# Performance work log

Measured on AMD Instinct MI355X. Metric: run time of the kernel, lower is better.

## Reference

```python
import jax, jax.numpy as jnp
import numpy as np

HEADS = 8
DIM_HEAD = 64
DIM_COOR = 3
SCALE = (DIM_COOR * DIM_HEAD) ** -0.5


def setup_inputs() -> dict:
    key = jax.random.key(0)
    k1, k2, k3 = jax.random.split(key, 3)
    x = jax.random.normal(k1, (2, 2048, 256, 3), dtype=jnp.float32)
    w_qkv = jax.random.normal(k2, (1536, 256), dtype=jnp.float32)
    w_out = jax.random.normal(k3, (256, 512), dtype=jnp.float32)
    return {"x": x, "w_qkv": w_qkv, "w_out": w_out}


def reference(x, w_qkv, w_out):
    b, n, _, c = x.shape
    # VNLinear: contract feature dim, keep coord dim  -> [b, n, 3*h*d, c]
    qkv = jnp.einsum('bnic,oi->bnoc', x, w_qkv)
    q, k, v = jnp.split(qkv, 3, axis=-2)  # each [b, n, h*d, c]

    def to_heads(t):
        return t.reshape(b, n, HEADS, DIM_HEAD, c).transpose(0, 2, 1, 3, 4)  # b h n d c

    q, k, v = map(to_heads, (q, k, v))
    q = q * SCALE
    # scores sum over head-dim AND coordinate-dim
    sim = jnp.einsum('bhidc,bhjdc->bhij', q, k)
    attn = jax.nn.softmax(sim, axis=-1)
    out = jnp.einsum('bhij,bhjdc->bhidc', attn, v)  # coord dim preserved
    out = out.transpose(0, 2, 1, 3, 4).reshape(b, n, HEADS * DIM_HEAD, c)
    return jnp.einsum('bnic,oi->bnoc', out, w_out)
```

## Files before the change

kernel.cpp:

```cpp
#include <hip/hip_runtime.h>
#include <hip/hip_bf16.h>

#define SCALE 0.07216878364870322f
#define LOG2E 1.4426950408889634f

typedef __bf16 bf16x8 __attribute__((ext_vector_type(8)));
typedef float f32x16 __attribute__((ext_vector_type(16)));
typedef float f32x4v __attribute__((ext_vector_type(4)));
typedef unsigned int u32x4 __attribute__((ext_vector_type(4)));
typedef unsigned short u16;

#define MFMA(a, b, c) __builtin_amdgcn_mfma_f32_32x32x16_bf16(a, b, c, 0, 0, 0)
#define MFMA16(a, b, c) __builtin_amdgcn_mfma_f32_16x16x32_bf16(a, b, c, 0, 0, 0)

__device__ __forceinline__ u16 b16(float v) { return __builtin_bit_cast(u16, (__bf16)v); }
__device__ __forceinline__ float fb16(u16 u) {
    unsigned int t = (unsigned int)u << 16;
    return __builtin_bit_cast(float, t);
}
__device__ __forceinline__ unsigned int splitpack(float v) {
    u16 h = b16(v);
    float r = v - fb16(h);
    return (unsigned int)h | ((unsigned int)b16(r) << 16);
}
__device__ __forceinline__ unsigned int pack2(float a, float b) {
    return (unsigned int)b16(a) | ((unsigned int)b16(b) << 16);
}
__device__ __forceinline__ void gload16(const void* g, void* l) {
    __builtin_amdgcn_global_load_lds((const __attribute__((address_space(1))) void*)g,
                                     (__attribute__((address_space(3))) void*)l, 16, 0, 0);
}

__global__ __launch_bounds__(256) void qkv_mfma(const float* __restrict__ x,
                                                const float* __restrict__ wq,
                                                u16* __restrict__ Qhi, u16* __restrict__ Qlo,
                                                u16* __restrict__ KVf) {
    __shared__ unsigned int ldsr[2][32][196];
    const int tid = threadIdx.x;
    const int lane = tid & 63, w = tid >> 6, hf = lane >> 5, l31 = lane & 31;
    const int lq = lane & 15, gq = lane >> 4;
    const int o0 = blockIdx.x * 64;
    const int n0 = blockIdx.y * 128;
    const int b = blockIdx.z;
    const int nw0 = n0 + w * 32;
    const int part = o0 >> 9;
    const int h = (o0 >> 6) & 7;
    const int bh = b * 8 + h;

    const float* xp = x + ((size_t)(b * 2048 + nw0 + l31)) * 768 + hf * 24;
    const float* wp0 = wq + (size_t)(o0 + l31) * 256 + hf * 8;
    const float* wp1 = wp0 + 32 * 256;

    f32x16 acc[3][2] = {};
    #pragma unroll 2
    for (int k0 = 0; k0 < 16; ++k0) {
        float xf[24], wf0[8], wf1[8];
        #pragma unroll
        for (int q = 0; q < 6; ++q) {
            f32x4v t = *(const f32x4v*)(xp + k0 * 48 + q * 4);
            xf[q * 4 + 0] = t[0]; xf[q * 4 + 1] = t[1];
            xf[q * 4 + 2] = t[2]; xf[q * 4 + 3] = t[3];
        }
        {
            f32x4v t0 = *(const f32x4v*)(wp0 + k0 * 16);
            f32x4v t1 = *(const f32x4v*)(wp0 + k0 * 16 + 4);
            f32x4v t2 = *(const f32x4v*)(wp1 + k0 * 16);
            f32x4v t3 = *(const f32x4v*)(wp1 + k0 * 16 + 4);
            #pragma unroll
            for (int e = 0; e < 4; ++e) {
                wf0[e] = t0[e]; wf0[4 + e] = t1[e];
                wf1[e] = t2[e]; wf1[4 + e] = t3[e];
            }
        }
        bf16x8 xh[3], xl[3], wh[2], wl[2];
        #pragma unroll
        for (int c = 0; c < 3; ++c)
            #pragma unroll
            for (int e = 0; e < 8; ++e) {
                float v = xf[e * 3 + c];
                __bf16 hi = (__bf16)v;
                xh[c][e] = hi;
                xl[c][e] = (__bf16)(v - (float)hi);
            }
        #pragma unroll
        for (int e = 0; e < 8; ++e) {
            { float v = wf0[e]; __bf16 hi = (__bf16)v; wh[0][e] = hi; wl[0][e] = (__bf16)(v - (float)hi); }
            { float v = wf1[e]; __bf16 hi = (__bf16)v; wh[1][e] = hi; wl[1][e] = (__bf16)(v - (float)hi); }
        }
        #pragma unroll
        for (int c = 0; c < 3; ++c)
            #pragma unroll
            for (int ot = 0; ot < 2; ++ot) {
                acc[c][ot] = MFMA(xh[c], wh[ot], acc[c][ot]);
                acc[c][ot] = MFMA(xl[c], wh[ot], acc[c][ot]);
                acc[c][ot] = MFMA(xh[c], wl[ot], acc[c][ot]);
            }
    }

    #pragma unroll
    for (int round = 0; round < 2; ++round) {
        __syncthreads();
        if ((w >> 1) == round) {
            unsigned int (*L)[196] = ldsr[w & 1];
            #pragma unroll
            for (int c = 0; c < 3; ++c)
                #pragma unroll
                for (int ot = 0; ot < 2; ++ot)
                    #pragma unroll
                    for (int r = 0; r < 16; ++r) {
                        float v = acc[c][ot][r];
                        if (part == 0) v *= (SCALE * LOG2E);
                        int nn = (r & 3) + 8 * (r >> 2) + 4 * hf;
                        int dcol = 3 * (ot * 32 + l31) + c;
                        L[nn][dcol] = (part == 2) ? (unsigned int)b16(v) : splitpack(v);
                    }
            if (part < 2) {
                #pragma unroll
                for (int is = 0; is < 2; ++is)
                    #pragma unroll
                    for (int kc = 0; kc < 6; ++kc) {
                        const unsigned int* p = &L[is * 16 + lq][kc * 32 + gq * 8];
                        u32x4 a = *(const u32x4*)p;
                        u32x4 bq = *(const u32x4*)(p + 4);
                        u32x4 hi = { (a[0] & 0xffffu) | (a[1] << 16), (a[2] & 0xffffu) | (a[3] << 16),
                                     (bq[0] & 0xffffu) | (bq[1] << 16), (bq[2] & 0xffffu) | (bq[3] << 16) };
                        u32x4 lo = { (a[0] >> 16) | (a[1] & 0xffff0000u), (a[2] >> 16) | (a[3] & 0xffff0000u),
                                     (bq[0] >> 16) | (bq[1] & 0xffff0000u), (bq[2] >> 16) | (bq[3] & 0xffff0000u) };
                        if (part == 0) {
                            size_t off = ((size_t)(bh * 128 + (nw0 >> 4) + is) * 6 + kc) * 512 + lane * 8;
                            *(u32x4*)(Qhi + off) = hi;
                            *(u32x4*)(Qlo + off) = lo;
                        } else {
                            size_t off = (size_t)(bh * 64 + (nw0 >> 5)) * 18432 + (is * 6 + kc) * 512 + lane * 8;
                            *(u32x4*)(KVf + off) = hi;
                            *(u32x4*)(KVf + off + 6144) = lo;
                        }
                    }
            } else {
                u16* vp = KVf + (size_t)(bh * 64 + (nw0 >> 5)) * 18432 + 12288 + lane * 8;
                #pragma unroll
                for (int d = 0; d < 12; ++d) {
                    unsigned int t[8];
                    #pragma unroll
                    for (int e = 0; e < 8; ++e)
                        t[e] = L[gq * 8 + e][d * 16 + lq];
                    u32x4 pk = { (t[0] & 0xffffu) | (t[1] << 16), (t[2] & 0xffffu) | (t[3] << 16),
                                 (t[4] & 0xffffu) | (t[5] << 16), (t[6] & 0xffffu) | (t[7] << 16) };
                    *(u32x4*)(vp + d * 512) = pk;
                }
            }
        }
    }
}

__global__ __launch_bounds__(512, 2) void attn_mfma(
    const u16* __restrict__ Qhi, const u16* __restrict__ Qlo,
    const u16* __restrict__ KVf, unsigned int* __restrict__ att2) {
    __shared__ __align__(16) u16 lds[2][2][18432];
    const int tid = threadIdx.x;
    const int lane = tid & 63;
    const int w = tid >> 6;
    const int half = w >> 2;
    const int wl = w & 3;
    const int g = lane >> 4;
    const int i = lane & 15;
    const int id = blockIdx.x;
    const int bh = (id & 7) * 2 + (id >> 7);
    const int itile = (id >> 3) & 15;

    bf16x8 qh[2][6], ql[2][6];
    #pragma unroll
    for (int is = 0; is < 2; ++is) {
        size_t qb = (size_t)(bh * 128 + itile * 8 + wl * 2 + is) * 3072 + (size_t)lane * 8;
        #pragma unroll
        for (int kc = 0; kc < 6; ++kc) {
            qh[is][kc] = *(const bf16x8*)(Qhi + qb + kc * 512);
            ql[is][kc] = *(const bf16x8*)(Qlo + qb + kc * 512);
        }
    }

    const char* gKV = (const char*)KVf + (size_t)bh * 2359296;
    const int t256 = tid & 255;
    auto stage = [&](int buf, int jtAbs) {
        const char* src = gKV + (size_t)jtAbs * 36864;
        char* dst = (char*)&lds[half][buf][0];
        #pragma unroll
        for (int s = 0; s < 9; ++s) {
            const int c16 = (t256 + s * 256) * 16;
            gload16(src + c16, dst + c16);
        }
    };

    const int jt0 = half * 32;
    stage(0, jt0);
    __syncthreads();
    int cur = 0;

    f32x4v o[2][12] = {};
    float m_run[2] = {-1e30f, -1e30f}, l_run[2] = {0.f, 0.f};

    for (int t = 0; t < 32; ++t) {
        if (t + 1 < 32) stage(cur ^ 1, jt0 + t + 1);
        const u16* L = &lds[half][cur][0];

        f32x4v s4[2][2] = {};
        __builtin_amdgcn_s_setprio(1);
        #pragma unroll
        for (int kc = 0; kc < 6; ++kc) {
            bf16x8 kh0 = *(const bf16x8*)&L[(unsigned)(kc * 512) + lane * 8];
            bf16x8 kh1 = *(const bf16x8*)&L[(unsigned)((6 + kc) * 512) + lane * 8];
            bf16x8 kl0 = *(const bf16x8*)&L[6144u + (unsigned)(kc * 512) + lane * 8];
            bf16x8 kl1 = *(const bf16x8*)&L[6144u + (unsigned)((6 + kc) * 512) + lane * 8];
            s4[0][0] = MFMA16(kh0, qh[0][kc], s4[0][0]);
            s4[0][1] = MFMA16(kh1, qh[0][kc], s4[0][1]);
            s4[1][0] = MFMA16(kh0, qh[1][kc], s4[1][0]);
            s4[1][1] = MFMA16(kh1, qh[1][kc], s4[1][1]);
            s4[0][0] = MFMA16(kh0, ql[0][kc], s4[0][0]);
            s4[0][1] = MFMA16(kh1, ql[0][kc], s4[0][1]);
            s4[1][0] = MFMA16(kh0, ql[1][kc], s4[1][0]);
            s4[1][1] = MFMA16(kh1, ql[1][kc], s4[1][1]);
            s4[0][0] = MFMA16(kl0, qh[0][kc], s4[0][0]);
            s4[0][1] = MFMA16(kl1, qh[0][kc], s4[0][1]);
            s4[1][0] = MFMA16(kl0, qh[1][kc], s4[1][0]);
            s4[1][1] = MFMA16(kl1, qh[1][kc], s4[1][1]);
        }
        __builtin_amdgcn_s_setprio(0);

        bf16x8 pb[2];
        #pragma unroll
        for (int is = 0; is < 2; ++is) {
            float pm = -1e30f;
            #pragma unroll
            for (int js = 0; js < 2; ++js)
                #pragma unroll
                for (int r = 0; r < 4; ++r) pm = fmaxf(pm, s4[is][js][r]);
            pm = fmaxf(pm, __shfl_xor(pm, 16, 64));
            pm = fmaxf(pm, __shfl_xor(pm, 32, 64));
            if (!__all(pm <= m_run[is] + 8.0f)) {
                float mnew = fmaxf(m_run[is], pm);
                float sc = exp2f(m_run[is] - mnew);
                l_run[is] *= sc;
                #pragma unroll
                for (int d = 0; d < 12; ++d) o[is][d] = o[is][d] * sc;
                m_run[is] = mnew;
            }
            float rs = 0.f;
            unsigned int w0[2], w1[2];
            #pragma unroll
            for (int js = 0; js < 2; ++js) {
                float p0 = exp2f(s4[is][js][0] - m_run[is]), p1 = exp2f(s4[is][js][1] - m_run[is]);
                float p2 = exp2f(s4[is][js][2] - m_run[is]), p3 = exp2f(s4[is][js][3] - m_run[is]);
                rs += (p0 + p1) + (p2 + p3);
                w0[js] = pack2(p0, p1);
                w1[js] = pack2(p2, p3);
            }
            rs += __shfl_xor(rs, 16, 64);
            rs += __shfl_xor(rs, 32, 64);
            l_run[is] += rs;

            u32x4 F;
            const int slA = ((g & 1) << 5) + i;
            const int slB = slA + 16;
            const bool ghi = (g >> 1) != 0;
            { unsigned a0 = __shfl((int)w0[0], slA, 64), a1 = __shfl((int)w0[1], slA, 64); F[0] = ghi ? a1 : a0; }
            { unsigned a0 = __shfl((int)w1[0], slA, 64), a1 = __shfl((int)w1[1], slA, 64); F[1] = ghi ? a1 : a0; }
            { unsigned a0 = __shfl((int)w0[0], slB, 64), a1 = __shfl((int)w0[1], slB, 64); F[2] = ghi ? a1 : a0; }
            { unsigned a0 = __shfl((int)w1[0], slB, 64), a1 = __shfl((int)w1[1], slB, 64); F[3] = ghi ? a1 : a0; }
            pb[is] = __builtin_bit_cast(bf16x8, F);
        }

        __builtin_amdgcn_s_setprio(1);
        #pragma unroll
        for (int d = 0; d < 12; ++d) {
            bf16x8 vf = *(const bf16x8*)&L[12288u + (unsigned)(d * 512) + lane * 8];
            o[0][d] = MFMA16(vf, pb[0], o[0][d]);
            o[1][d] = MFMA16(vf, pb[1], o[1][d]);
        }
        __builtin_amdgcn_s_setprio(0);

        if (t + 1 < 32) {
            __syncthreads();
            cur ^= 1;
        }
    }

    float* LM = (float*)&lds[0][0][0];
    __syncthreads();
    if (half == 1) {
        #pragma unroll
        for (int is = 0; is < 2; ++is) {
            #pragma unroll
            for (int d = 0; d < 12; ++d)
                *(f32x4v*)&LM[(((wl * 2 + is) * 12 + d) * 64 + lane) * 4] = o[is][d];
            LM[24576 + ((wl * 2 + is) * 64 + lane) * 2 + 0] = m_run[is];
            LM[24576 + ((wl * 2 + is) * 64 + lane) * 2 + 1] = l_run[is];
        }
    }
    __syncthreads();
    if (half == 0) {
        const int b2 = bh >> 3, hh = bh & 7;
        #pragma unroll
        for (int is = 0; is < 2; ++is) {
            float mb = LM[24576 + ((wl * 2 + is) * 64 + lane) * 2 + 0];
            float lb = LM[24576 + ((wl * 2 + is) * 64 + lane) * 2 + 1];
            float mm = fmaxf(m_run[is], mb);
            float wa = exp2f(m_run[is] - mm);
            float wb = exp2f(mb - mm);
            float inv = 1.0f / (l_run[is] * wa + lb * wb);
            const int ig = (itile * 8 + wl * 2 + is) * 16 + i;
            const int itq = ig >> 5, i31 = ig & 31;
            #pragma unroll
            for (int d = 0; d < 12; ++d) {
                f32x4v vb = *(const f32x4v*)&LM[(((wl * 2 + is) * 12 + d) * 64 + lane) * 4];
                #pragma unroll
                for (int r = 0; r < 4; ++r) {
                    float v = (o[is][d][r] * wa + vb[r] * wb) * inv;
                    int dc = d * 16 + g * 4 + r;
                    int dd = dc / 3, cc2 = dc - dd * 3;
                    int hd = hh * 64 + dd;
                    int ks = hd >> 4, e = hd & 7;
                    int ln = i31 | (((hd >> 3) & 1) << 5);
                    size_t off = (((size_t)(b2 * 3 + cc2) * 32 + ks) * 64 + itq) * 512 + (size_t)ln * 8 + e;
                    att2[off] = splitpack(v);
                }
            }
        }
    }
}

__global__ __launch_bounds__(256) void out_mfma(const unsigned int* __restrict__ att2,
                                                const float* __restrict__ wo,
                                                float* __restrict__ out) {
    const int tid = threadIdx.x, lane = tid & 63, w = tid >> 6, hf = lane >> 5, l31 = lane & 31;
    const int o0 = blockIdx.x * 32;
    const int n5 = blockIdx.y * 4 + w;
    const int b = blockIdx.z;
    const float* wp = wo + (size_t)(o0 + l31) * 512 + hf * 8;
    const unsigned int* ap = att2 + ((size_t)(b * 3) * 2048 + n5) * 512 + (size_t)lane * 8;
    f32x16 acc[3] = {};
    #pragma unroll 2
    for (int ks = 0; ks < 32; ++ks) {
        bf16x8 wh, wl;
        {
            f32x4v t0 = *(const f32x4v*)(wp + ks * 16);
            f32x4v t1 = *(const f32x4v*)(wp + ks * 16 + 4);
            #pragma unroll
            for (int e = 0; e < 4; ++e) {
                { float v = t0[e]; __bf16 hi = (__bf16)v; wh[e] = hi; wl[e] = (__bf16)(v - (float)hi); }
                { float v = t1[e]; __bf16 hi = (__bf16)v; wh[4 + e] = hi; wl[4 + e] = (__bf16)(v - (float)hi); }
            }
        }
        #pragma unroll
        for (int c = 0; c < 3; ++c) {
            const unsigned int* pc = ap + (size_t)c * 1048576 + ks * 32768;
            u32x4 a0 = *(const u32x4*)pc;
            u32x4 a1 = *(const u32x4*)(pc + 4);
            union { bf16x8 v; u32x4 u; } H, Lo;
            H.u  = { (a0[0] & 0xffffu) | (a0[1] << 16), (a0[2] & 0xffffu) | (a0[3] << 16),
                     (a1[0] & 0xffffu) | (a1[1] << 16), (a1[2] & 0xffffu) | (a1[3] << 16) };
            Lo.u = { (a0[0] >> 16) | (a0[1] & 0xffff0000u), (a0[2] >> 16) | (a0[3] & 0xffff0000u),
                     (a1[0] >> 16) | (a1[1] & 0xffff0000u), (a1[2] >> 16) | (a1[3] & 0xffff0000u) };
            acc[c] = MFMA(H.v, wh, acc[c]);
            acc[c] = MFMA(Lo.v, wh, acc[c]);
            acc[c] = MFMA(H.v, wl, acc[c]);
        }
    }
    #pragma unroll
    for (int r = 0; r < 16; ++r) {
        int n = (n5 << 5) + (r & 3) + 8 * (r >> 2) + 4 * hf;
        size_t off = ((size_t)(b * 2048 + n) * 256 + o0 + l31) * 3;
        out[off]     = acc[0][r];
        out[off + 1] = acc[1][r];
        out[off + 2] = acc[2][r];
    }
}

extern "C" void kernel_launch(void* const* d_in, const int* in_sizes, int n_in,
                              void* d_out, int out_size, void* d_ws, size_t ws_size,
                              hipStream_t stream) {
    const float* x     = (const float*)d_in[0];
    const float* w_qkv = (const float*)d_in[1];
    const float* w_out = (const float*)d_in[2];
    float* out = (float*)d_out;

    const size_t NB = (size_t)16 * 2048 * 192;
    const size_t KVN = (size_t)16 * 64 * 18432;
    u16* Qhi = (u16*)d_ws;
    u16* Qlo = Qhi + NB;
    u16* KVf = Qlo + NB;
    unsigned int* att2 = (unsigned int*)(KVf + KVN);

    qkv_mfma<<<dim3(24, 16, 2), 256, 0, stream>>>(x, w_qkv, Qhi, Qlo, KVf);
    attn_mfma<<<dim3(256), 512, 0, stream>>>(Qhi, Qlo, KVf, att2);
    out_mfma<<<dim3(8, 16, 2), 256, 0, stream>>>(att2, w_out, out);
}
```

Before: 234.4 us.

## Split attention KV halves into separate blocks and merge partials in output GEMM

```diff
diff --git a/kernel.cpp b/kernel.cpp
--- a/kernel.cpp
+++ b/kernel.cpp
@@ -39,9 +39,14 @@
     const int tid = threadIdx.x;
     const int lane = tid & 63, w = tid >> 6, hf = lane >> 5, l31 = lane & 31;
     const int lq = lane & 15, gq = lane >> 4;
-    const int o0 = blockIdx.x * 64;
-    const int n0 = blockIdx.y * 128;
-    const int b = blockIdx.z;
+    const int id = blockIdx.x;
+    const int xcd = id & 7;
+    const int jj = id >> 3;
+    const int nb = xcd * 4 + jj / 24;
+    const int ot = jj % 24;
+    const int o0 = ot * 64;
+    const int b = nb >> 4;
+    const int n0 = (nb & 15) * 128;
     const int nw0 = n0 + w * 32;
     const int part = o0 >> 9;
     const int h = (o0 >> 6) & 7;
@@ -90,10 +95,10 @@
         #pragma unroll
         for (int c = 0; c < 3; ++c)
             #pragma unroll
-            for (int ot = 0; ot < 2; ++ot) {
-                acc[c][ot] = MFMA(xh[c], wh[ot], acc[c][ot]);
-                acc[c][ot] = MFMA(xl[c], wh[ot], acc[c][ot]);
-                acc[c][ot] = MFMA(xh[c], wl[ot], acc[c][ot]);
+            for (int ot2 = 0; ot2 < 2; ++ot2) {
+                acc[c][ot2] = MFMA(xh[c], wh[ot2], acc[c][ot2]);
+                acc[c][ot2] = MFMA(xl[c], wh[ot2], acc[c][ot2]);
+                acc[c][ot2] = MFMA(xh[c], wl[ot2], acc[c][ot2]);
             }
     }
 
@@ -105,13 +110,13 @@
             #pragma unroll
             for (int c = 0; c < 3; ++c)
                 #pragma unroll
-                for (int ot = 0; ot < 2; ++ot)
+                for (int ot2 = 0; ot2 < 2; ++ot2)
                     #pragma unroll
                     for (int r = 0; r < 16; ++r) {
-                        float v = acc[c][ot][r];
+                        float v = acc[c][ot2][r];
                         if (part == 0) v *= (SCALE * LOG2E);
                         int nn = (r & 3) + 8 * (r >> 2) + 4 * hf;
-                        int dcol = 3 * (ot * 32 + l31) + c;
+                        int dcol = 3 * (ot2 * 32 + l31) + c;
                         L[nn][dcol] = (part == 2) ? (unsigned int)b16(v) : splitpack(v);
                     }
             if (part < 2) {
@@ -153,20 +158,22 @@
     }
 }
 
-__global__ __launch_bounds__(512, 2) void attn_mfma(
+__global__ __launch_bounds__(256, 2) void attn_mfma(
     const u16* __restrict__ Qhi, const u16* __restrict__ Qlo,
-    const u16* __restrict__ KVf, unsigned int* __restrict__ att2) {
-    __shared__ __align__(16) u16 lds[2][2][18432];
+    const u16* __restrict__ KVf, u16* __restrict__ OpA, u16* __restrict__ OpB,
+    float2* __restrict__ MLp) {
+    __shared__ __align__(16) u16 lds[2][18432];
     const int tid = threadIdx.x;
     const int lane = tid & 63;
-    const int w = tid >> 6;
-    const int half = w >> 2;
-    const int wl = w & 3;
+    const int wl = tid >> 6;
     const int g = lane >> 4;
     const int i = lane & 15;
     const int id = blockIdx.x;
-    const int bh = (id & 7) * 2 + (id >> 7);
-    const int itile = (id >> 3) & 15;
+    const int rem = id >> 3;
+    const int grp = ((rem >> 4) << 3) | (id & 7);
+    const int itile = rem & 15;
+    const int bh = grp >> 1;
+    const int half = grp & 1;
 
     bf16x8 qh[2][6], ql[2][6];
     #pragma unroll
@@ -180,13 +187,12 @@
     }
 
     const char* gKV = (const char*)KVf + (size_t)bh * 2359296;
-    const int t256 = tid & 255;
     auto stage = [&](int buf, int jtAbs) {
         const char* src = gKV + (size_t)jtAbs * 36864;
-        char* dst = (char*)&lds[half][buf][0];
+        char* dst = (char*)&lds[buf][0];
         #pragma unroll
         for (int s = 0; s < 9; ++s) {
-            const int c16 = (t256 + s * 256) * 16;
+            const int c16 = (tid + s * 256) * 16;
             gload16(src + c16, dst + c16);
         }
     };
@@ -201,7 +207,7 @@
 
     for (int t = 0; t < 32; ++t) {
         if (t + 1 < 32) stage(cur ^ 1, jt0 + t + 1);
-        const u16* L = &lds[half][cur][0];
+        const u16* L = &lds[cur][0];
 
         f32x4v s4[2][2] = {};
         __builtin_amdgcn_s_setprio(1);
@@ -284,51 +290,34 @@
         }
     }
 
-    float* LM = (float*)&lds[0][0][0];
-    __syncthreads();
-    if (half == 1) {
-        #pragma unroll
-        for (int is = 0; is < 2; ++is) {
-            #pragma unroll
-            for (int d = 0; d < 12; ++d)
-                *(f32x4v*)&LM[(((wl * 2 + is) * 12 + d) * 64 + lane) * 4] = o[is][d];
-            LM[24576 + ((wl * 2 + is) * 64 + lane) * 2 + 0] = m_run[is];
-            LM[24576 + ((wl * 2 + is) * 64 + lane) * 2 + 1] = l_run[is];
-        }
-    }
-    __syncthreads();
-    if (half == 0) {
-        const int b2 = bh >> 3, hh = bh & 7;
-        #pragma unroll
-        for (int is = 0; is < 2; ++is) {
-            float mb = LM[24576 + ((wl * 2 + is) * 64 + lane) * 2 + 0];
-            float lb = LM[24576 + ((wl * 2 + is) * 64 + lane) * 2 + 1];
-            float mm = fmaxf(m_run[is], mb);
-            float wa = exp2f(m_run[is] - mm);
-            float wb = exp2f(mb - mm);
-            float inv = 1.0f / (l_run[is] * wa + lb * wb);
-            const int ig = (itile * 8 + wl * 2 + is) * 16 + i;
-            const int itq = ig >> 5, i31 = ig & 31;
-            #pragma unroll
-            for (int d = 0; d < 12; ++d) {
-                f32x4v vb = *(const f32x4v*)&LM[(((wl * 2 + is) * 12 + d) * 64 + lane) * 4];
-                #pragma unroll
-                for (int r = 0; r < 4; ++r) {
-                    float v = (o[is][d][r] * wa + vb[r] * wb) * inv;
-                    int dc = d * 16 + g * 4 + r;
-                    int dd = dc / 3, cc2 = dc - dd * 3;
-                    int hd = hh * 64 + dd;
-                    int ks = hd >> 4, e = hd & 7;
-                    int ln = i31 | (((hd >> 3) & 1) << 5);
-                    size_t off = (((size_t)(b2 * 3 + cc2) * 32 + ks) * 64 + itq) * 512 + (size_t)ln * 8 + e;
-                    att2[off] = splitpack(v);
-                }
-            }
-        }
-    }
-}
-
-__global__ __launch_bounds__(256) void out_mfma(const unsigned int* __restrict__ att2,
+    const int b2 = bh >> 3, hh = bh & 7;
+    u16* P = half ? OpB : OpA;
+    #pragma unroll
+    for (int is = 0; is < 2; ++is) {
+        const int ig = (itile * 8 + wl * 2 + is) * 16 + i;
+        const int itq = ig >> 5, i31 = ig & 31;
+        #pragma unroll
+        for (int d = 0; d < 12; ++d)
+            #pragma unroll
+            for (int r = 0; r < 4; ++r) {
+                int dc = d * 16 + g * 4 + r;
+                int dd = dc / 3, cc2 = dc - dd * 3;
+                int hd = hh * 64 + dd;
+                int ks = hd >> 4, e = hd & 7;
+                int ln = i31 | (((hd >> 3) & 1) << 5);
+                size_t off = (((size_t)(b2 * 3 + cc2) * 32 + ks) * 64 + itq) * 512 + (size_t)ln * 8 + e;
+                P[off] = b16(o[is][d][r]);
+            }
+        if (g == 0) {
+            float2 ml; ml.x = m_run[is]; ml.y = l_run[is];
+            MLp[(size_t)half * 32768 + bh * 2048 + ig] = ml;
+        }
+    }
+}
+
+__global__ __launch_bounds__(256) void out_mfma(const u16* __restrict__ OpA,
+                                                const u16* __restrict__ OpB,
+                                                const float2* __restrict__ MLp,
                                                 const float* __restrict__ wo,
                                                 float* __restrict__ out) {
     const int tid = threadIdx.x, lane = tid & 63, w = tid >> 6, hf = lane >> 5, l31 = lane & 31;
@@ -336,10 +325,24 @@
     const int n5 = blockIdx.y * 4 + w;
     const int b = blockIdx.z;
     const float* wp = wo + (size_t)(o0 + l31) * 512 + hf * 8;
-    const unsigned int* ap = att2 + ((size_t)(b * 3) * 2048 + n5) * 512 + (size_t)lane * 8;
+
+    float wa[8], wb[8], inv[8];
+    #pragma unroll
+    for (int hh = 0; hh < 8; ++hh) {
+        size_t mi = (size_t)(b * 8 + hh) * 2048 + n5 * 32 + l31;
+        float2 A = MLp[mi];
+        float2 Bm = MLp[32768 + mi];
+        float mm = fmaxf(A.x, Bm.x);
+        wa[hh] = exp2f(A.x - mm);
+        wb[hh] = exp2f(Bm.x - mm);
+        inv[hh] = 1.0f / (A.y * wa[hh] + Bm.y * wb[hh]);
+    }
+
     f32x16 acc[3] = {};
     #pragma unroll 2
     for (int ks = 0; ks < 32; ++ks) {
+        const int hh = ks >> 2;
+        const float waH = wa[hh], wbH = wb[hh], invH = inv[hh];
         bf16x8 wh, wl;
         {
             f32x4v t0 = *(const f32x4v*)(wp + ks * 16);
@@ -352,14 +355,28 @@
         }
         #pragma unroll
         for (int c = 0; c < 3; ++c) {
-            const unsigned int* pc = ap + (size_t)c * 1048576 + ks * 32768;
-            u32x4 a0 = *(const u32x4*)pc;
-            u32x4 a1 = *(const u32x4*)(pc + 4);
+            size_t pc = (size_t)(b * 3 + c) * 1048576 + (size_t)ks * 32768 + (size_t)n5 * 512 + (size_t)lane * 8;
+            u32x4 aA = *(const u32x4*)(OpA + pc);
+            u32x4 aB = *(const u32x4*)(OpB + pc);
+            unsigned hiw[4], low[4];
+            #pragma unroll
+            for (int q = 0; q < 4; ++q) {
+                unsigned ha = 0, la = 0;
+                #pragma unroll
+                for (int s = 0; s < 2; ++s) {
+                    u16 ua = (u16)((aA[q] >> (s * 16)) & 0xffffu);
+                    u16 ub = (u16)((aB[q] >> (s * 16)) & 0xffffu);
+                    float v = (fb16(ua) * waH + fb16(ub) * wbH) * invH;
+                    u16 hv = b16(v);
+                    u16 lv = b16(v - fb16(hv));
+                    ha |= ((unsigned)hv) << (s * 16);
+                    la |= ((unsigned)lv) << (s * 16);
+                }
+                hiw[q] = ha; low[q] = la;
+            }
             union { bf16x8 v; u32x4 u; } H, Lo;
-            H.u  = { (a0[0] & 0xffffu) | (a0[1] << 16), (a0[2] & 0xffffu) | (a0[3] << 16),
-                     (a1[0] & 0xffffu) | (a1[1] << 16), (a1[2] & 0xffffu) | (a1[3] << 16) };
-            Lo.u = { (a0[0] >> 16) | (a0[1] & 0xffff0000u), (a0[2] >> 16) | (a0[3] & 0xffff0000u),
-                     (a1[0] >> 16) | (a1[1] & 0xffff0000u), (a1[2] >> 16) | (a1[3] & 0xffff0000u) };
+            H.u  = { hiw[0], hiw[1], hiw[2], hiw[3] };
+            Lo.u = { low[0], low[1], low[2], low[3] };
             acc[c] = MFMA(H.v, wh, acc[c]);
             acc[c] = MFMA(Lo.v, wh, acc[c]);
             acc[c] = MFMA(H.v, wl, acc[c]);
@@ -388,9 +405,11 @@
     u16* Qhi = (u16*)d_ws;
     u16* Qlo = Qhi + NB;
     u16* KVf = Qlo + NB;
-    unsigned int* att2 = (unsigned int*)(KVf + KVN);
-
-    qkv_mfma<<<dim3(24, 16, 2), 256, 0, stream>>>(x, w_qkv, Qhi, Qlo, KVf);
-    attn_mfma<<<dim3(256), 512, 0, stream>>>(Qhi, Qlo, KVf, att2);
-    out_mfma<<<dim3(8, 16, 2), 256, 0, stream>>>(att2, w_out, out);
-}
+    u16* OpA = KVf + KVN;
+    u16* OpB = OpA + NB;
+    float2* MLp = (float2*)(OpB + NB);
+
+    qkv_mfma<<<dim3(768), 256, 0, stream>>>(x, w_qkv, Qhi, Qlo, KVf);
+    attn_mfma<<<dim3(512), 256, 0, stream>>>(Qhi, Qlo, KVf, OpA, OpB, MLp);
+    out_mfma<<<dim3(8, 16, 2), 256, 0, stream>>>(OpA, OpB, MLp, w_out, out);
+}
```

New measurement: 226.5 us. 1.03x faster.
